# Kernel tuning notes

Hardware: AMD Instinct MI355X
Metric: run time of the kernel (lower is better)

Reference implementation:

```python
import jax, jax.numpy as jnp
import numpy as np

IN_FEATURES = 4096
OUT_FEATURES = 4096
NNZ = 838860
BATCH = 512


def setup_inputs() -> dict:
    key = jax.random.key(0)
    kx, kr, kc, kv, kb = jax.random.split(key, 5)
    x = jax.random.normal(kx, (BATCH, IN_FEATURES), dtype=jnp.float32)
    row_idx = jax.random.randint(kr, (NNZ,), 0, OUT_FEATURES, dtype=jnp.int64)
    col_idx = jax.random.randint(kc, (NNZ,), 0, IN_FEATURES, dtype=jnp.int64)
    values = jax.random.normal(kv, (NNZ,), dtype=jnp.float32)
    bias = jax.random.normal(kb, (OUT_FEATURES,), dtype=jnp.float32)
    return {"x": x, "row_idx": row_idx, "col_idx": col_idx,
            "values": values, "bias": bias}


def reference(x, row_idx, col_idx, values, bias):
    # COO sparse linear: y[b, row] += x[b, col] * val, then add bias.
    x_flat = x.reshape(-1, IN_FEATURES)                    # [B, in]
    weighted = x_flat[:, col_idx] * values                 # [B, nnz]
    out = jnp.zeros((x_flat.shape[0], OUT_FEATURES), dtype=x.dtype)
    out = out.at[:, row_idx].add(weighted)                 # scatter-add per row
    out = out + bias
    return out.reshape(x.shape[:-1] + (OUT_FEATURES,))
```

## Files before the change

kernel.cpp:

```cpp
#include <hip/hip_runtime.h>

#define IN_F    4096
#define OUT_F   4096
#define K_DIM   4096
#define NNZ_C   838860
#define BATCH   512
#define BK      32
#define BM      128
#define BN      128

typedef short bf16x8 __attribute__((ext_vector_type(8)));
typedef float f32x4  __attribute__((ext_vector_type(4)));

__device__ __forceinline__ unsigned short f2bf(float f) {
    unsigned u = __float_as_uint(f);
    u += 0x7fffu + ((u >> 16) & 1u);
    return (unsigned short)(u >> 16);
}
__device__ __forceinline__ void gload_lds16(const void* g, void* l) {
    __builtin_amdgcn_global_load_lds(
        (const __attribute__((address_space(1))) unsigned int*)g,
        (__attribute__((address_space(3))) unsigned int*)l, 16, 0, 0);
}

#define N_WZ   (OUT_F * K_DIM / 8)
#define N_CVT  (BATCH * K_DIM / 8)
#define N_OUT  (BATCH * OUT_F / 4)
__global__ void prep(const float* __restrict__ x,
                     unsigned short* __restrict__ xb,
                     const float* __restrict__ bias,
                     float* __restrict__ out,
                     uint4* __restrict__ Wz, int do_bias) {
    int i = blockIdx.x * 256 + threadIdx.x;
    if (i < N_WZ) { Wz[i] = make_uint4(0, 0, 0, 0); return; }
    i -= N_WZ;
    if (i < N_CVT) {
        const float4* p = (const float4*)x + (size_t)i * 2;
        float4 a = p[0], b = p[1];
        union { unsigned short h[8]; bf16x8 v; } u;
        u.h[0] = f2bf(a.x); u.h[1] = f2bf(a.y); u.h[2] = f2bf(a.z); u.h[3] = f2bf(a.w);
        u.h[4] = f2bf(b.x); u.h[5] = f2bf(b.y); u.h[6] = f2bf(b.z); u.h[7] = f2bf(b.w);
        ((bf16x8*)xb)[i] = u.v;
        return;
    }
    i -= N_CVT;
    if (i < N_OUT && do_bias) {
        float4 b = ((const float4*)bias)[i & (OUT_F / 4 - 1)];
        ((float4*)out)[i] = b;
    }
}
#define PREP_BLOCKS ((N_WZ + N_CVT + N_OUT) / 256)

__global__ void scatter_pk(const int* __restrict__ row_idx,
                           const int* __restrict__ col_idx,
                           const float* __restrict__ values,
                           unsigned short* __restrict__ W) {
    int i = blockIdx.x * 256 + threadIdx.x;
    if (i >= NNZ_C / 4) return;
    int4   r4 = ((const int4*)row_idx)[i];
    int4   c4 = ((const int4*)col_idx)[i];
    float4 v4 = ((const float4*)values)[i];
#pragma unroll
    for (int j = 0; j < 4; ++j) {
        int r = (&r4.x)[j], c = (&c4.x)[j];
        float v = (&v4.x)[j];
        unsigned idx = (unsigned)r * K_DIM + (unsigned)c;
        unsigned short h = f2bf(v);
        unsigned data = (idx & 1u) ? ((unsigned)h << 16) : (unsigned)h;
        unsigned long long addr = (unsigned long long)(W + (idx & ~1u));
        asm volatile("global_atomic_pk_add_bf16 %0, %1, off"
                     :: "v"(addr), "v"(data) : "memory");
    }
}

template <int EPI, int SK>
__global__ void __launch_bounds__(256)
gemm_bt(const unsigned short* __restrict__ Abf,
        const unsigned short* __restrict__ Wbf,
        const float* __restrict__ bias,
        float* __restrict__ out,
        float* __restrict__ parts) {
    __shared__ __align__(16) unsigned short As[BM * BK];
    __shared__ __align__(16) unsigned short Bs[BN * BK];

    const int nt = blockIdx.x, mt = blockIdx.y, s = blockIdx.z;
    const int t = threadIdx.x, w = t >> 6, ln = t & 63;
    const int wm = w & 1, wn = w >> 1;
    const int KSs = K_DIM / SK;
    const int ks0 = s * KSs;

    const int srow = w * 16 + (ln >> 2);
    const int scol = (((ln & 3) ^ ((ln >> 3) & 3)) * 8);
    const unsigned short* gA0 = Abf + (size_t)(mt * BM + srow) * K_DIM + ks0 + scol;
    const unsigned short* gA1 = gA0 + (size_t)64 * K_DIM;
    const unsigned short* gB0 = Wbf + (size_t)(nt * BN + srow) * K_DIM + ks0 + scol;
    const unsigned short* gB1 = gB0 + (size_t)64 * K_DIM;
    unsigned short* lA0 = &As[(w * 16) * BK];
    unsigned short* lA1 = &As[(64 + w * 16) * BK];
    unsigned short* lB0 = &Bs[(w * 16) * BK];
    unsigned short* lB1 = &Bs[(64 + w * 16) * BK];

    const int quad = ln >> 4, lanem = ln & 15;
    const int rsw = (quad ^ ((lanem >> 1) & 3)) * 8;
    const unsigned short* rA = &As[(wm * 64 + lanem) * BK + rsw];
    const unsigned short* rB = &Bs[(wn * 64 + lanem) * BK + rsw];

    f32x4 acc[4][4];
#pragma unroll
    for (int mi = 0; mi < 4; ++mi)
#pragma unroll
        for (int ni = 0; ni < 4; ++ni)
            acc[mi][ni] = (f32x4){0.f, 0.f, 0.f, 0.f};

    for (int kt = 0; kt < KSs / BK; ++kt) {
        __syncthreads();
        gload_lds16(gA0 + kt * BK, lA0);
        gload_lds16(gA1 + kt * BK, lA1);
        gload_lds16(gB0 + kt * BK, lB0);
        gload_lds16(gB1 + kt * BK, lB1);
        __syncthreads();

        bf16x8 af[4], bfr[4];
#pragma unroll
        for (int mi = 0; mi < 4; ++mi) af[mi]  = *(const bf16x8*)(rA + mi * 16 * BK);
#pragma unroll
        for (int ni = 0; ni < 4; ++ni) bfr[ni] = *(const bf16x8*)(rB + ni * 16 * BK);
#pragma unroll
        for (int mi = 0; mi < 4; ++mi)
#pragma unroll
            for (int ni = 0; ni < 4; ++ni)
                acc[mi][ni] = __builtin_amdgcn_mfma_f32_16x16x32_bf16(
                    af[mi], bfr[ni], acc[mi][ni], 0, 0, 0);
    }

    const int row0 = mt * BM + wm * 64 + quad * 4;
    const int col0 = nt * BN + wn * 64 + lanem;
    if (EPI == 0) {
        float bv[4];
#pragma unroll
        for (int ni = 0; ni < 4; ++ni) bv[ni] = (s == 0) ? bias[col0 + ni * 16] : 0.f;
        float* dst = (s == 0) ? out : parts + (size_t)(s - 1) * BATCH * OUT_F;
#pragma unroll
        for (int mi = 0; mi < 4; ++mi)
#pragma unroll
            for (int ni = 0; ni < 4; ++ni)
#pragma unroll
                for (int r = 0; r < 4; ++r)
                    dst[(size_t)(row0 + mi * 16 + r) * OUT_F + col0 + ni * 16] =
                        acc[mi][ni][r] + bv[ni];
    } else {
#pragma unroll
        for (int mi = 0; mi < 4; ++mi)
#pragma unroll
            for (int ni = 0; ni < 4; ++ni)
#pragma unroll
                for (int r = 0; r < 4; ++r)
                    atomicAdd(&out[(size_t)(row0 + mi * 16 + r) * OUT_F + col0 + ni * 16],
                              acc[mi][ni][r]);
    }
}

__global__ void reduce_parts(float* __restrict__ out,
                             const float* __restrict__ parts) {
    int i = blockIdx.x * 256 + threadIdx.x;
    float4 a = ((const float4*)out)[i];
#pragma unroll
    for (int p = 0; p < 7; ++p) {
        float4 b = ((const float4*)(parts + (size_t)p * BATCH * OUT_F))[i];
        a.x += b.x; a.y += b.y; a.z += b.z; a.w += b.w;
    }
    ((float4*)out)[i] = a;
}

extern "C" void kernel_launch(void* const* d_in, const int* in_sizes, int n_in,
                              void* d_out, int out_size, void* d_ws, size_t ws_size,
                              hipStream_t stream) {
    const float* x       = (const float*)d_in[0];
    const int*   row_idx = (const int*)d_in[1];
    const int*   col_idx = (const int*)d_in[2];
    const float* values  = (const float*)d_in[3];
    const float* bias    = (const float*)d_in[4];
    float*       out     = (float*)d_out;

    unsigned short* xb = (unsigned short*)d_ws;
    unsigned short* W  = xb + (size_t)BATCH * K_DIM;
    float* parts = (float*)(W + (size_t)OUT_F * K_DIM);
    size_t need = (size_t)BATCH * K_DIM * 2 + (size_t)OUT_F * K_DIM * 2
                + (size_t)7 * BATCH * OUT_F * 4;
    bool use_parts = (ws_size >= need);

    prep<<<PREP_BLOCKS, 256, 0, stream>>>(x, xb, bias, out, (uint4*)W,
                                          use_parts ? 0 : 1);
    scatter_pk<<<(NNZ_C / 4 + 255) / 256, 256, 0, stream>>>(
        row_idx, col_idx, values, W);

    if (use_parts) {
        gemm_bt<0, 8><<<dim3(OUT_F / BN, BATCH / BM, 8), 256, 0, stream>>>(
            xb, W, bias, out, parts);
        reduce_parts<<<BATCH * OUT_F / 4 / 256, 256, 0, stream>>>(out, parts);
    } else {
        gemm_bt<1, 4><<<dim3(OUT_F / BN, BATCH / BM, 4), 256, 0, stream>>>(
            xb, W, bias, out, nullptr);
    }
}
```

Before: 163.0 us.

## Fuse prep, scatter, GEMM and reduction into one persistent kernel with grid barriers

Replaces the four separate launches (zero/convert, scatter, split-K GEMM, reduce) with one persistent 1024-block kernel. Software grid barriers separate the phases, and scatter runs alongside the x conversion by splitting blocks between the two jobs. The aim is to remove launch gaps and tail idle time between kernels. In exchange it depends on all 1024 blocks being co-resident (checked through the occupancy API). It also adds a memset and barrier spin costs, and the barrier could deadlock if co-residency is misjudged.

```diff
diff --git a/kernel.cpp b/kernel.cpp
--- a/kernel.cpp
+++ b/kernel.cpp
@@ -8,6 +8,11 @@
 #define BK      32
 #define BM      128
 #define BN      128
+#define NBLK    1024
+#define SCAT_BLKS 820
+#define CVT_BLKS  (NBLK - SCAT_BLKS)
+#define N_CVT   (BATCH * K_DIM / 8)
+#define N_RED   (BATCH * OUT_F / 4)
 
 typedef short bf16x8 __attribute__((ext_vector_type(8)));
 typedef float f32x4  __attribute__((ext_vector_type(4)));
@@ -22,15 +27,189 @@
         (const __attribute__((address_space(1))) unsigned int*)g,
         (__attribute__((address_space(3))) unsigned int*)l, 16, 0, 0);
 }
+__device__ __forceinline__ void pk_add(unsigned short* W, int r, int c, float v) {
+    unsigned idx = (unsigned)r * K_DIM + (unsigned)c;
+    unsigned short h = f2bf(v);
+    unsigned data = (idx & 1u) ? ((unsigned)h << 16) : (unsigned)h;
+    unsigned long long addr = (unsigned long long)(W + (idx & ~1u));
+    asm volatile("global_atomic_pk_add_bf16 %0, %1, off"
+                 :: "v"(addr), "v"(data) : "memory");
+}
+
+__device__ __forceinline__ void grid_bar(int* cnt, int* gen) {
+    __syncthreads();
+    if (threadIdx.x == 0) {
+        __threadfence();
+        int g = __hip_atomic_load(gen, __ATOMIC_RELAXED, __HIP_MEMORY_SCOPE_AGENT);
+        int v = __hip_atomic_fetch_add(cnt, 1, __ATOMIC_ACQ_REL, __HIP_MEMORY_SCOPE_AGENT);
+        if (v == NBLK - 1) {
+            __hip_atomic_store(cnt, 0, __ATOMIC_RELAXED, __HIP_MEMORY_SCOPE_AGENT);
+            __hip_atomic_fetch_add(gen, 1, __ATOMIC_ACQ_REL, __HIP_MEMORY_SCOPE_AGENT);
+        } else {
+            while (__hip_atomic_load(gen, __ATOMIC_ACQUIRE, __HIP_MEMORY_SCOPE_AGENT) == g)
+                __builtin_amdgcn_s_sleep(2);
+        }
+    }
+    __syncthreads();
+}
+
+template <int EPI, int SK>
+__device__ __forceinline__ void gemm_body(
+    int nt, int mt, int s, int t,
+    const unsigned short* __restrict__ Abf,
+    const unsigned short* __restrict__ Wbf,
+    const float* __restrict__ bias,
+    float* __restrict__ out, float* __restrict__ parts,
+    unsigned short* As, unsigned short* Bs) {
+    const int w = t >> 6, ln = t & 63;
+    const int wm = w & 1, wn = w >> 1;
+    const int KSs = K_DIM / SK;
+    const int ks0 = s * KSs;
+
+    const int srow = w * 16 + (ln >> 2);
+    const int scol = (((ln & 3) ^ ((ln >> 3) & 3)) * 8);
+    const unsigned short* gA0 = Abf + (size_t)(mt * BM + srow) * K_DIM + ks0 + scol;
+    const unsigned short* gA1 = gA0 + (size_t)64 * K_DIM;
+    const unsigned short* gB0 = Wbf + (size_t)(nt * BN + srow) * K_DIM + ks0 + scol;
+    const unsigned short* gB1 = gB0 + (size_t)64 * K_DIM;
+    unsigned short* lA0 = &As[(w * 16) * BK];
+    unsigned short* lA1 = &As[(64 + w * 16) * BK];
+    unsigned short* lB0 = &Bs[(w * 16) * BK];
+    unsigned short* lB1 = &Bs[(64 + w * 16) * BK];
+
+    const int quad = ln >> 4, lanem = ln & 15;
+    const int rsw = (quad ^ ((lanem >> 1) & 3)) * 8;
+    const unsigned short* rA = &As[(wm * 64 + lanem) * BK + rsw];
+    const unsigned short* rB = &Bs[(wn * 64 + lanem) * BK + rsw];
+
+    f32x4 acc[4][4];
+#pragma unroll
+    for (int mi = 0; mi < 4; ++mi)
+#pragma unroll
+        for (int ni = 0; ni < 4; ++ni)
+            acc[mi][ni] = (f32x4){0.f, 0.f, 0.f, 0.f};
+
+    for (int kt = 0; kt < KSs / BK; ++kt) {
+        __syncthreads();
+        gload_lds16(gA0 + kt * BK, lA0);
+        gload_lds16(gA1 + kt * BK, lA1);
+        gload_lds16(gB0 + kt * BK, lB0);
+        gload_lds16(gB1 + kt * BK, lB1);
+        __syncthreads();
+
+        bf16x8 af[4], bfr[4];
+#pragma unroll
+        for (int mi = 0; mi < 4; ++mi) af[mi]  = *(const bf16x8*)(rA + mi * 16 * BK);
+#pragma unroll
+        for (int ni = 0; ni < 4; ++ni) bfr[ni] = *(const bf16x8*)(rB + ni * 16 * BK);
+#pragma unroll
+        for (int mi = 0; mi < 4; ++mi)
+#pragma unroll
+            for (int ni = 0; ni < 4; ++ni)
+                acc[mi][ni] = __builtin_amdgcn_mfma_f32_16x16x32_bf16(
+                    af[mi], bfr[ni], acc[mi][ni], 0, 0, 0);
+    }
+
+    const int row0 = mt * BM + wm * 64 + quad * 4;
+    const int col0 = nt * BN + wn * 64 + lanem;
+    if (EPI == 0) {
+        float bv[4];
+#pragma unroll
+        for (int ni = 0; ni < 4; ++ni) bv[ni] = (s == 0) ? bias[col0 + ni * 16] : 0.f;
+        float* dst = (s == 0) ? out : parts + (size_t)(s - 1) * BATCH * OUT_F;
+#pragma unroll
+        for (int mi = 0; mi < 4; ++mi)
+#pragma unroll
+            for (int ni = 0; ni < 4; ++ni)
+#pragma unroll
+                for (int r = 0; r < 4; ++r)
+                    dst[(size_t)(row0 + mi * 16 + r) * OUT_F + col0 + ni * 16] =
+                        acc[mi][ni][r] + bv[ni];
+    } else {
+#pragma unroll
+        for (int mi = 0; mi < 4; ++mi)
+#pragma unroll
+            for (int ni = 0; ni < 4; ++ni)
+#pragma unroll
+                for (int r = 0; r < 4; ++r)
+                    atomicAdd(&out[(size_t)(row0 + mi * 16 + r) * OUT_F + col0 + ni * 16],
+                              acc[mi][ni][r]);
+    }
+}
+
+__global__ void __launch_bounds__(256, 4)
+fused(const float* __restrict__ x,
+      const int* __restrict__ row_idx,
+      const int* __restrict__ col_idx,
+      const float* __restrict__ values,
+      const float* __restrict__ bias,
+      float* __restrict__ out,
+      int* __restrict__ bar,
+      unsigned short* __restrict__ xb,
+      unsigned short* __restrict__ W,
+      float* __restrict__ parts) {
+    __shared__ __align__(16) unsigned short As[BM * BK];
+    __shared__ __align__(16) unsigned short Bs[BN * BK];
+    const int b = blockIdx.x, t = threadIdx.x;
+    const int gtid = b * 256 + t;
+
+    {
+        uint4* Wz = (uint4*)W;
+#pragma unroll
+        for (int j = 0; j < 8; ++j)
+            Wz[(size_t)gtid + (size_t)j * (NBLK * 256)] = make_uint4(0, 0, 0, 0);
+    }
+    grid_bar(bar, bar + 64);
+
+    if (b < SCAT_BLKS) {
+        int i = gtid;
+        if (i < NNZ_C / 4) {
+            int4   r4 = ((const int4*)row_idx)[i];
+            int4   c4 = ((const int4*)col_idx)[i];
+            float4 v4 = ((const float4*)values)[i];
+            pk_add(W, r4.x, c4.x, v4.x);
+            pk_add(W, r4.y, c4.y, v4.y);
+            pk_add(W, r4.z, c4.z, v4.z);
+            pk_add(W, r4.w, c4.w, v4.w);
+        }
+    } else {
+        for (int j = (b - SCAT_BLKS) * 256 + t; j < N_CVT; j += CVT_BLKS * 256) {
+            const float4* p = (const float4*)x + (size_t)j * 2;
+            float4 a = p[0], bb = p[1];
+            union { unsigned short h[8]; bf16x8 v; } u;
+            u.h[0] = f2bf(a.x);  u.h[1] = f2bf(a.y);
+            u.h[2] = f2bf(a.z);  u.h[3] = f2bf(a.w);
+            u.h[4] = f2bf(bb.x); u.h[5] = f2bf(bb.y);
+            u.h[6] = f2bf(bb.z); u.h[7] = f2bf(bb.w);
+            ((bf16x8*)xb)[j] = u.v;
+        }
+    }
+    grid_bar(bar, bar + 64);
+
+    gemm_body<0, 8>(b & 31, (b >> 5) & 3, b >> 7, t, xb, W, bias, out, parts,
+                    As, Bs);
+    grid_bar(bar, bar + 64);
+
+#pragma unroll
+    for (int j = 0; j < 2; ++j) {
+        size_t i = (size_t)gtid + (size_t)j * (NBLK * 256);
+        float4 a = ((const float4*)out)[i];
+#pragma unroll
+        for (int p = 0; p < 7; ++p) {
+            float4 v = ((const float4*)(parts + (size_t)p * BATCH * OUT_F))[i];
+            a.x += v.x; a.y += v.y; a.z += v.z; a.w += v.w;
+        }
+        ((float4*)out)[i] = a;
+    }
+}
 
 #define N_WZ   (OUT_F * K_DIM / 8)
-#define N_CVT  (BATCH * K_DIM / 8)
 #define N_OUT  (BATCH * OUT_F / 4)
 __global__ void prep(const float* __restrict__ x,
                      unsigned short* __restrict__ xb,
                      const float* __restrict__ bias,
                      float* __restrict__ out,
-                     uint4* __restrict__ Wz, int do_bias) {
+                     uint4* __restrict__ Wz) {
     int i = blockIdx.x * 256 + threadIdx.x;
     if (i < N_WZ) { Wz[i] = make_uint4(0, 0, 0, 0); return; }
     i -= N_WZ;
@@ -44,13 +223,11 @@
         return;
     }
     i -= N_CVT;
-    if (i < N_OUT && do_bias) {
+    if (i < N_OUT) {
         float4 b = ((const float4*)bias)[i & (OUT_F / 4 - 1)];
         ((float4*)out)[i] = b;
     }
 }
-#define PREP_BLOCKS ((N_WZ + N_CVT + N_OUT) / 256)
-
 __global__ void scatter_pk(const int* __restrict__ row_idx,
                            const int* __restrict__ col_idx,
                            const float* __restrict__ values,
@@ -60,116 +237,20 @@
     int4   r4 = ((const int4*)row_idx)[i];
     int4   c4 = ((const int4*)col_idx)[i];
     float4 v4 = ((const float4*)values)[i];
-#pragma unroll
-    for (int j = 0; j < 4; ++j) {
-        int r = (&r4.x)[j], c = (&c4.x)[j];
-        float v = (&v4.x)[j];
-        unsigned idx = (unsigned)r * K_DIM + (unsigned)c;
-        unsigned short h = f2bf(v);
-        unsigned data = (idx & 1u) ? ((unsigned)h << 16) : (unsigned)h;
-        unsigned long long addr = (unsigned long long)(W + (idx & ~1u));
-        asm volatile("global_atomic_pk_add_bf16 %0, %1, off"
-                     :: "v"(addr), "v"(data) : "memory");
-    }
-}
-
-template <int EPI, int SK>
+    pk_add(W, r4.x, c4.x, v4.x);
+    pk_add(W, r4.y, c4.y, v4.y);
+    pk_add(W, r4.z, c4.z, v4.z);
+    pk_add(W, r4.w, c4.w, v4.w);
+}
 __global__ void __launch_bounds__(256)
-gemm_bt(const unsigned short* __restrict__ Abf,
-        const unsigned short* __restrict__ Wbf,
-        const float* __restrict__ bias,
-        float* __restrict__ out,
-        float* __restrict__ parts) {
+gemm_atomic(const unsigned short* __restrict__ Abf,
+            const unsigned short* __restrict__ Wbf,
+            const float* __restrict__ bias,
+            float* __restrict__ out) {
     __shared__ __align__(16) unsigned short As[BM * BK];
     __shared__ __align__(16) unsigned short Bs[BN * BK];
-
-    const int nt = blockIdx.x, mt = blockIdx.y, s = blockIdx.z;
-    const int t = threadIdx.x, w = t >> 6, ln = t & 63;
-    const int wm = w & 1, wn = w >> 1;
-    const int KSs = K_DIM / SK;
-    const int ks0 = s * KSs;
-
-    const int srow = w * 16 + (ln >> 2);
-    const int scol = (((ln & 3) ^ ((ln >> 3) & 3)) * 8);
-    const unsigned short* gA0 = Abf + (size_t)(mt * BM + srow) * K_DIM + ks0 + scol;
-    const unsigned short* gA1 = gA0 + (size_t)64 * K_DIM;
-    const unsigned short* gB0 = Wbf + (size_t)(nt * BN + srow) * K_DIM + ks0 + scol;
-    const unsigned short* gB1 = gB0 + (size_t)64 * K_DIM;
-    unsigned short* lA0 = &As[(w * 16) * BK];
-    unsigned short* lA1 = &As[(64 + w * 16) * BK];
-    unsigned short* lB0 = &Bs[(w * 16) * BK];
-    unsigned short* lB1 = &Bs[(64 + w * 16) * BK];
-
-    const int quad = ln >> 4, lanem = ln & 15;
-    const int rsw = (quad ^ ((lanem >> 1) & 3)) * 8;
-    const unsigned short* rA = &As[(wm * 64 + lanem) * BK + rsw];
-    const unsigned short* rB = &Bs[(wn * 64 + lanem) * BK + rsw];
-
-    f32x4 acc[4][4];
-#pragma unroll
-    for (int mi = 0; mi < 4; ++mi)
-#pragma unroll
-        for (int ni = 0; ni < 4; ++ni)
-            acc[mi][ni] = (f32x4){0.f, 0.f, 0.f, 0.f};
-
-    for (int kt = 0; kt < KSs / BK; ++kt) {
-        __syncthreads();
-        gload_lds16(gA0 + kt * BK, lA0);
-        gload_lds16(gA1 + kt * BK, lA1);
-        gload_lds16(gB0 + kt * BK, lB0);
-        gload_lds16(gB1 + kt * BK, lB1);
-        __syncthreads();
-
-        bf16x8 af[4], bfr[4];
-#pragma unroll
-        for (int mi = 0; mi < 4; ++mi) af[mi]  = *(const bf16x8*)(rA + mi * 16 * BK);
-#pragma unroll
-        for (int ni = 0; ni < 4; ++ni) bfr[ni] = *(const bf16x8*)(rB + ni * 16 * BK);
-#pragma unroll
-        for (int mi = 0; mi < 4; ++mi)
-#pragma unroll
-            for (int ni = 0; ni < 4; ++ni)
-                acc[mi][ni] = __builtin_amdgcn_mfma_f32_16x16x32_bf16(
-                    af[mi], bfr[ni], acc[mi][ni], 0, 0, 0);
-    }
-
-    const int row0 = mt * BM + wm * 64 + quad * 4;
-    const int col0 = nt * BN + wn * 64 + lanem;
-    if (EPI == 0) {
-        float bv[4];
-#pragma unroll
-        for (int ni = 0; ni < 4; ++ni) bv[ni] = (s == 0) ? bias[col0 + ni * 16] : 0.f;
-        float* dst = (s == 0) ? out : parts + (size_t)(s - 1) * BATCH * OUT_F;
-#pragma unroll
-        for (int mi = 0; mi < 4; ++mi)
-#pragma unroll
-            for (int ni = 0; ni < 4; ++ni)
-#pragma unroll
-                for (int r = 0; r < 4; ++r)
-                    dst[(size_t)(row0 + mi * 16 + r) * OUT_F + col0 + ni * 16] =
-                        acc[mi][ni][r] + bv[ni];
-    } else {
-#pragma unroll
-        for (int mi = 0; mi < 4; ++mi)
-#pragma unroll
-            for (int ni = 0; ni < 4; ++ni)
-#pragma unroll
-                for (int r = 0; r < 4; ++r)
-                    atomicAdd(&out[(size_t)(row0 + mi * 16 + r) * OUT_F + col0 + ni * 16],
-                              acc[mi][ni][r]);
-    }
-}
-
-__global__ void reduce_parts(float* __restrict__ out,
-                             const float* __restrict__ parts) {
-    int i = blockIdx.x * 256 + threadIdx.x;
-    float4 a = ((const float4*)out)[i];
-#pragma unroll
-    for (int p = 0; p < 7; ++p) {
-        float4 b = ((const float4*)(parts + (size_t)p * BATCH * OUT_F))[i];
-        a.x += b.x; a.y += b.y; a.z += b.z; a.w += b.w;
-    }
-    ((float4*)out)[i] = a;
+    gemm_body<1, 4>(blockIdx.x, blockIdx.y, blockIdx.z, threadIdx.x,
+                    Abf, Wbf, bias, out, nullptr, As, Bs);
 }
 
 extern "C" void kernel_launch(void* const* d_in, const int* in_sizes, int n_in,
@@ -182,24 +263,28 @@
     const float* bias    = (const float*)d_in[4];
     float*       out     = (float*)d_out;
 
-    unsigned short* xb = (unsigned short*)d_ws;
+    int* bar = (int*)d_ws;
+    unsigned short* xb = (unsigned short*)((char*)d_ws + 256);
     unsigned short* W  = xb + (size_t)BATCH * K_DIM;
     float* parts = (float*)(W + (size_t)OUT_F * K_DIM);
-    size_t need = (size_t)BATCH * K_DIM * 2 + (size_t)OUT_F * K_DIM * 2
+    size_t need = 256 + (size_t)BATCH * K_DIM * 2 + (size_t)OUT_F * K_DIM * 2
                 + (size_t)7 * BATCH * OUT_F * 4;
-    bool use_parts = (ws_size >= need);
-
-    prep<<<PREP_BLOCKS, 256, 0, stream>>>(x, xb, bias, out, (uint4*)W,
-                                          use_parts ? 0 : 1);
-    scatter_pk<<<(NNZ_C / 4 + 255) / 256, 256, 0, stream>>>(
-        row_idx, col_idx, values, W);
-
-    if (use_parts) {
-        gemm_bt<0, 8><<<dim3(OUT_F / BN, BATCH / BM, 8), 256, 0, stream>>>(
-            xb, W, bias, out, parts);
-        reduce_parts<<<BATCH * OUT_F / 4 / 256, 256, 0, stream>>>(out, parts);
+
+    int maxb = 0;
+    hipError_t e = hipOccupancyMaxActiveBlocksPerMultiprocessor(
+        &maxb, (const void*)fused, 256, 0);
+    bool coop = (e == hipSuccess) && (maxb >= 4) && (ws_size >= need);
+
+    if (coop) {
+        hipMemsetAsync(bar, 0, 256, stream);
+        fused<<<NBLK, 256, 0, stream>>>(x, row_idx, col_idx, values, bias,
+                                        out, bar, xb, W, parts);
     } else {
-        gemm_bt<1, 4><<<dim3(OUT_F / BN, BATCH / BM, 4), 256, 0, stream>>>(
-            xb, W, bias, out, nullptr);
-    }
-}
+        prep<<<(N_WZ + N_CVT + N_OUT) / 256, 256, 0, stream>>>(
+            x, xb, bias, out, (uint4*)W);
+        scatter_pk<<<(NNZ_C / 4 + 255) / 256, 256, 0, stream>>>(
+            row_idx, col_idx, values, W);
+        gemm_atomic<<<dim3(OUT_F / BN, BATCH / BM, 4), 256, 0, stream>>>(
+            xb, W, bias, out);
+    }
+}
```

Result: slower. 169.4 us (+4.0%).
